# Kernel optimization log

Hardware: AMD Instinct MI355X
Metric: run time of the kernel (lower is better)

Reference implementation:

```python
import jax, jax.numpy as jnp
import numpy as np

A = 20000        # distinct library arcs
T = 500000       # timing arcs in design
S = 8            # LUT slew-axis length
C = 8            # LUT load-axis length
G = 250000       # gates
TOTAL_U = 1000000  # gate x candidate-master entries
SCALE = 1.0e15
MAX_CAP = 1.0e-12
MAX_ITER = 3


def _axis_interval(ax, x):
    """ax: [M,K] monotone axes, x: [M]. Returns lower index i0 in [0,K-2] and frac a (may extrapolate)."""
    K = ax.shape[1]
    i0 = jnp.clip(jnp.sum(ax <= x[:, None], axis=1) - 1, 0, K - 2)
    ar = jnp.arange(ax.shape[0])
    x0 = ax[ar, i0]
    x1 = ax[ar, i0 + 1]
    a = (x - x0) / (x1 - x0)
    return i0, a


def _bilinear_gate(in_slew, load, dtab, stab, axs, axc):
    """Batched bilinear interpolation into per-arc 2D LUTs. All leading dims M."""
    M = in_slew.shape[0]
    ar = jnp.arange(M)
    i0, a = _axis_interval(axs, in_slew)
    j0, b = _axis_interval(axc, load)
    i1, j1 = i0 + 1, j0 + 1

    def _blerp(t):
        return ((1 - a) * (1 - b) * t[ar, i0, j0]
                + (1 - a) * b * t[ar, i0, j1]
                + a * (1 - b) * t[ar, i1, j0]
                + a * b * t[ar, i1, j1])

    return _blerp(dtab), _blerp(stab)


def _compute_ceff_batch(in_slew, c1, c2, rpi, dtab, stab, axs, axc, max_iter=MAX_ITER):
    ceff = jnp.maximum(c1 + c2, 1e-30)
    for _ in range(max_iter):
        d, _ = _bilinear_gate(in_slew, ceff, dtab, stab, axs, axc)
        tau = jnp.maximum(d, 1e-30)
        ratio = jnp.minimum(2.0 * tau / jnp.maximum(in_slew, 1e-30), 10.0)
        h = jnp.where(ratio > 0.01, (1.0 - jnp.exp(-ratio)) / ratio, 1.0 - ratio / 2.0)
        ceff = jnp.maximum(c1 + c2 * h, 1e-30)
    return ceff


def _segment_softmax(logits, gate_id, num_groups):
    """Numerically stable per-gate softmax via segment reductions."""
    gmax = jax.ops.segment_max(logits, gate_id, num_segments=num_groups)
    ex = jnp.exp(logits - gmax[gate_id])
    gsum = jax.ops.segment_sum(ex, gate_id, num_segments=num_groups)
    return ex / gsum[gate_id]


def _gate_grouped_forward(in_arr, in_slew, c1, c2, rpi, arc_idx_r, arc_idx_f,
                          unateness, delay_table, slew_table, load_index, slew_index):
    t = arc_idx_r.shape[0]
    arc_flat = jnp.stack([arc_idx_r, arc_idx_f], axis=1).reshape(-1)  # [2T]
    una = unateness[arc_flat]
    is_fall = jnp.arange(2 * t, dtype=una.dtype) % 2
    rf_idx = (una ^ is_fall).reshape(t, 2)  # rise/fall select per column
    in_slew_sel = jnp.take_along_axis(in_slew, rf_idx, axis=1).reshape(-1)
    in_arr_sel = jnp.take_along_axis(in_arr, rf_idx, axis=1).reshape(-1)

    dtab = delay_table[arc_flat]   # [2T,S,C] big gather (memory bound)
    stab = slew_table[arc_flat]
    axc = load_index[arc_flat]     # [2T,C]
    axs = slew_index[arc_flat]     # [2T,S]

    c1_f = jnp.repeat(c1, 2) / SCALE
    c2_f = jnp.repeat(c2, 2) / SCALE
    rpi_f = jnp.repeat(rpi, 2)
    load = _compute_ceff_batch(in_slew_sel, c1_f, c2_f, rpi_f, dtab, stab, axs, axc)
    load = jnp.minimum(load, MAX_CAP)

    arc_delay, arc_slew = _bilinear_gate(in_slew_sel, load, dtab, stab, axs, axc)
    arr_out = (in_arr_sel + arc_delay).reshape(t, 2)
    slew_out = arc_slew.reshape(t, 2)
    return jnp.concatenate([arr_out, slew_out], axis=1)  # [T,4]


def setup_inputs() -> dict:
    key = jax.random.key(0)
    ks = jax.random.split(key, 14)
    U_flat = jax.random.normal(ks[0], (TOTAL_U,), jnp.float32)
    gate_id = jnp.sort(jax.random.randint(ks[1], (TOTAL_U,), 0, G, dtype=jnp.int32))
    in_arr = jax.random.normal(ks[2], (T, 2), jnp.float32)
    in_slew = jax.random.uniform(ks[3], (T, 2), jnp.float32, 0.05, 3.0)
    c1 = jax.random.uniform(ks[4], (T,), jnp.float32, 0.0, 1.0)
    c2 = jax.random.uniform(ks[5], (T,), jnp.float32, 0.0, 1.0)
    rpi = jax.random.uniform(ks[6], (T,), jnp.float32, 0.1, 1.0)
    arc_idx_r = jax.random.randint(ks[7], (T,), 0, A, dtype=jnp.int32)
    arc_idx_f = jax.random.randint(ks[8], (T,), 0, A, dtype=jnp.int32)
    unateness = jax.random.randint(ks[9], (A,), 0, 2, dtype=jnp.int32)
    delay_table = jax.random.uniform(ks[10], (A, S, C), jnp.float32, 0.01, 1.0)
    slew_table = jax.random.uniform(ks[11], (A, S, C), jnp.float32, 0.01, 1.0)
    # strictly increasing LUT axes: slew axis ~[0.05, 4], load axis ~[5e-17, 3e-15]
    slew_index = jnp.cumsum(jax.random.uniform(ks[12], (A, S), jnp.float32, 0.05, 0.6), axis=1)
    load_index = jnp.cumsum(jax.random.uniform(ks[13], (A, C), jnp.float32, 0.05, 0.6), axis=1) * 1e-15
    return dict(U_flat=U_flat, gate_id=gate_id, in_arr=in_arr, in_slew=in_slew,
                c1=c1, c2=c2, rpi=rpi, arc_idx_r=arc_idx_r, arc_idx_f=arc_idx_f,
                unateness=unateness, delay_table=delay_table, slew_table=slew_table,
                slew_index=slew_index, load_index=load_index)


def reference(U_flat, gate_id, in_arr, in_slew, c1, c2, rpi, arc_idx_r, arc_idx_f,
              unateness, delay_table, slew_table, slew_index, load_index):
    weights = _segment_softmax(U_flat, gate_id, G)  # per-gate soft master selection
    out = _gate_grouped_forward(in_arr, in_slew, c1, c2, rpi, arc_idx_r, arc_idx_f,
                                unateness, delay_table, slew_table, load_index, slew_index)
    return out, weights
```

## Files before the change

### kernel.cpp

```cpp
#include <hip/hip_runtime.h>

#define T_N 500000
#define U_N 1000000
#define G_N 250000
#define A_N 20000

#define SBLK 256
#define HALO 96

__device__ __forceinline__ float sel8(const float (&r)[8], int j) {
    float v = r[0];
#pragma unroll
    for (int k = 1; k < 8; ++k) v = (j >= k) ? r[k] : v;
    return v;
}

__device__ __forceinline__ void load8(const float* __restrict__ p, float (&r)[8]) {
    const float4* q = (const float4*)p;
    float4 a = q[0], b = q[1];
    r[0]=a.x; r[1]=a.y; r[2]=a.z; r[3]=a.w;
    r[4]=b.x; r[5]=b.y; r[6]=b.z; r[7]=b.w;
}


__global__ void __launch_bounds__(256)
softmax_lds_kernel(const float* __restrict__ U,
                   const int* __restrict__ gid,
                   float* __restrict__ wout) {
    __shared__ float se[SBLK + 2 * HALO];
    __shared__ int   sg[SBLK + 2 * HALO];

    int base = blockIdx.x * SBLK;
    int wstart = base - HALO;

    for (int k = threadIdx.x; k < SBLK + 2 * HALO; k += SBLK) {
        int idx = wstart + k;
        if (idx >= 0 && idx < U_N) {
            se[k] = expf(U[idx]);
            sg[k] = gid[idx];
        } else {
            se[k] = 0.0f;
            sg[k] = -1 - k;
        }
    }
    __syncthreads();

    int i = base + threadIdx.x;
    if (i >= U_N) return;

    int li = threadIdx.x + HALO;
    int g = sg[li];
    float mye = se[li];
    float s = mye;
    for (int j = li - 1; j >= 0 && sg[j] == g; --j) s += se[j];
    for (int j = li + 1; j < SBLK + 2 * HALO && sg[j] == g; ++j) s += se[j];

    wout[i] = mye / s;
}


__global__ void __launch_bounds__(256)
timing_kernel(const float2* __restrict__ in_arr,
              const float2* __restrict__ in_slew,
              const float* __restrict__ c1,
              const float* __restrict__ c2,
              const int* __restrict__ arc_r,
              const int* __restrict__ arc_f,
              const int* __restrict__ una,
              const float* __restrict__ dtab,
              const float* __restrict__ stab,
              const float* __restrict__ sidx,
              const float* __restrict__ lidx,
              float4* __restrict__ out)
{
    int t = blockIdx.x * blockDim.x + threadIdx.x;
    if (t >= T_N) return;

    float2 ia = in_arr[t];
    float2 is = in_slew[t];
    float c1f = c1[t] / 1.0e15f;
    float c2f = c2[t] / 1.0e15f;
    int arcs0 = arc_r[t];
    int arcs1 = arc_f[t];

    float res_arr[2], res_slew[2];

#pragma unroll
    for (int col = 0; col < 2; ++col) {
        int arc = (col == 0) ? arcs0 : arcs1;
        int u   = una[arc];
        int rf  = u ^ col;
        float slew = rf ? is.y : is.x;
        float arr  = rf ? ia.y : ia.x;

        float s[8], cx[8];
        load8(sidx + (size_t)arc * 8, s);
        load8(lidx + (size_t)arc * 8, cx);

        int cnt = 0;
#pragma unroll
        for (int k = 0; k < 8; ++k) cnt += (s[k] <= slew) ? 1 : 0;
        int i0 = min(max(cnt - 1, 0), 6);
        float x0 = sel8(s, i0);
        float x1 = sel8(s, i0 + 1);
        float a = (slew - x0) / (x1 - x0);
        float om_a = 1.0f - a;

        float d0[8], d1[8];
        load8(dtab + (size_t)arc * 64 + (size_t)i0 * 8, d0);
        load8(dtab + (size_t)arc * 64 + (size_t)i0 * 8 + 8, d1);

        float slew_den = fmaxf(slew, 1e-30f);
        float ceff = fmaxf(c1f + c2f, 1e-30f);
#pragma unroll
        for (int it = 0; it < 3; ++it) {
            int jc = 0;
#pragma unroll
            for (int k = 0; k < 8; ++k) jc += (cx[k] <= ceff) ? 1 : 0;
            int j0 = min(max(jc - 1, 0), 6);
            float y0 = sel8(cx, j0);
            float y1 = sel8(cx, j0 + 1);
            float b = (ceff - y0) / (y1 - y0);
            float om_b = 1.0f - b;
            float v00 = sel8(d0, j0), v01 = sel8(d0, j0 + 1);
            float v10 = sel8(d1, j0), v11 = sel8(d1, j0 + 1);
            float d = om_a * om_b * v00 + om_a * b * v01
                    + a * om_b * v10 + a * b * v11;
            float tau = fmaxf(d, 1e-30f);
            float ratio = fminf(2.0f * tau / slew_den, 10.0f);
            float h = (ratio > 0.01f) ? (1.0f - expf(-ratio)) / ratio
                                      : 1.0f - 0.5f * ratio;
            ceff = fmaxf(c1f + c2f * h, 1e-30f);
        }
        float load = fminf(ceff, 1.0e-12f);

        int jc = 0;
#pragma unroll
        for (int k = 0; k < 8; ++k) jc += (cx[k] <= load) ? 1 : 0;
        int j0 = min(max(jc - 1, 0), 6);
        float y0 = sel8(cx, j0);
        float y1 = sel8(cx, j0 + 1);
        float b = (load - y0) / (y1 - y0);
        float om_b = 1.0f - b;

        float v00 = sel8(d0, j0), v01 = sel8(d0, j0 + 1);
        float v10 = sel8(d1, j0), v11 = sel8(d1, j0 + 1);
        float delay = om_a * om_b * v00 + om_a * b * v01
                    + a * om_b * v10 + a * b * v11;

        const float* srow = stab + (size_t)arc * 64 + (size_t)i0 * 8;
        float s00 = srow[j0],     s01 = srow[j0 + 1];
        float s10 = srow[8 + j0], s11 = srow[8 + j0 + 1];
        float sl = om_a * om_b * s00 + om_a * b * s01
                 + a * om_b * s10 + a * b * s11;

        res_arr[col]  = arr + delay;
        res_slew[col] = sl;
    }

    out[t] = make_float4(res_arr[0], res_arr[1], res_slew[0], res_slew[1]);
}

extern "C" void kernel_launch(void* const* d_in, const int* in_sizes, int n_in,
                              void* d_out, int out_size, void* d_ws, size_t ws_size,
                              hipStream_t stream) {
    const float*  U      = (const float*)d_in[0];
    const int*    gid    = (const int*)d_in[1];
    const float2* in_arr = (const float2*)d_in[2];
    const float2* in_slw = (const float2*)d_in[3];
    const float*  c1     = (const float*)d_in[4];
    const float*  c2     = (const float*)d_in[5];
    const int*    arc_r  = (const int*)d_in[7];
    const int*    arc_f  = (const int*)d_in[8];
    const int*    una    = (const int*)d_in[9];
    const float*  dtab   = (const float*)d_in[10];
    const float*  stab   = (const float*)d_in[11];
    const float*  sidx   = (const float*)d_in[12];
    const float*  lidx   = (const float*)d_in[13];

    float* out  = (float*)d_out;
    float* wout = out + (size_t)T_N * 4;

    softmax_lds_kernel<<<(U_N + SBLK - 1) / SBLK, SBLK, 0, stream>>>(U, gid, wout);

    timing_kernel<<<(T_N + 255) / 256, 256, 0, stream>>>(
        in_arr, in_slw, c1, c2, arc_r, arc_f, una, dtab, stab, sidx, lidx,
        (float4*)out);
}
```

Before: 172.1 us.

## Sort timing arcs by library arc via histogram/scan/scatter before LUT evaluation

Adds a counting-sort pipeline (histogram, single-block scan, atomic scatter) that groups the 2T arc evaluations by library arc index and packs per-item inputs into a workspace. A new kernel then evaluates each item in sorted order, so neighbouring threads read the same LUT rows and gather-load locality improves. The cost is four extra launches, global atomics, a serial single-block scan, extra workspace traffic, and scattered 4-byte output writes. The original kernel is kept as a fallback when the workspace is too small.

```diff
diff --git a/kernel.cpp b/kernel.cpp
--- a/kernel.cpp
+++ b/kernel.cpp
@@ -4,6 +4,7 @@
 #define U_N 1000000
 #define G_N 250000
 #define A_N 20000
+#define ITEMS (2 * T_N)
 
 #define SBLK 256
 #define HALO 96
@@ -56,6 +57,161 @@
     for (int j = li + 1; j < SBLK + 2 * HALO && sg[j] == g; ++j) s += se[j];
 
     wout[i] = mye / s;
+}
+
+
+__global__ void hist_zero_kernel(int* __restrict__ hist) {
+    int i = blockIdx.x * blockDim.x + threadIdx.x;
+    if (i < A_N) hist[i] = 0;
+}
+
+__global__ void hist_kernel(const int* __restrict__ arc_r,
+                            const int* __restrict__ arc_f,
+                            int* __restrict__ hist) {
+    int i = blockIdx.x * blockDim.x + threadIdx.x;
+    if (i >= ITEMS) return;
+    int t = i >> 1;
+    int arc = (i & 1) ? arc_f[t] : arc_r[t];
+    atomicAdd(&hist[arc], 1);
+}
+
+__global__ void __launch_bounds__(1024)
+scan_kernel(const int* __restrict__ hist, int* __restrict__ ofs) {
+    __shared__ int part[1024];
+    const int CHUNK = (A_N + 1023) / 1024;
+    int tid = threadIdx.x;
+    int beg = tid * CHUNK;
+    int end = min(beg + CHUNK, A_N);
+    int s = 0;
+    for (int k = beg; k < end; ++k) s += hist[k];
+    part[tid] = s;
+    __syncthreads();
+    for (int off = 1; off < 1024; off <<= 1) {
+        int v = (tid >= off) ? part[tid - off] : 0;
+        __syncthreads();
+        part[tid] += v;
+        __syncthreads();
+    }
+    int run = (tid > 0) ? part[tid - 1] : 0;
+    for (int k = beg; k < end; ++k) { ofs[k] = run; run += hist[k]; }
+}
+
+__global__ void __launch_bounds__(256)
+scatter_kernel(const int* __restrict__ arc_r,
+               const int* __restrict__ arc_f,
+               const int* __restrict__ una,
+               const float2* __restrict__ in_arr,
+               const float2* __restrict__ in_slew,
+               const float* __restrict__ c1,
+               const float* __restrict__ c2,
+               int* __restrict__ ofs,
+               uint2* __restrict__ meta,
+               float4* __restrict__ vals) {
+    int i = blockIdx.x * blockDim.x + threadIdx.x;
+    if (i >= ITEMS) return;
+    int t   = i >> 1;
+    int col = i & 1;
+    int arc = col ? arc_f[t] : arc_r[t];
+    int pos = atomicAdd(&ofs[arc], 1);
+
+    float2 ia = in_arr[t];
+    float2 is = in_slew[t];
+    int rf = una[arc] ^ col;
+    float arr  = rf ? ia.y : ia.x;
+    float slew = rf ? is.y : is.x;
+    float c1f = c1[t] / 1.0e15f;
+    float c2f = c2[t] / 1.0e15f;
+
+    meta[pos] = make_uint2((unsigned)i, (unsigned)arc);
+    vals[pos] = make_float4(arr, slew, c1f, c2f);
+}
+
+
+__global__ void __launch_bounds__(256)
+timing_sorted_kernel(const uint2* __restrict__ meta,
+                     const float4* __restrict__ vals,
+                     const float* __restrict__ dtab,
+                     const float* __restrict__ stab,
+                     const float* __restrict__ sidx,
+                     const float* __restrict__ lidx,
+                     float* __restrict__ out) {
+    int p = blockIdx.x * blockDim.x + threadIdx.x;
+    if (p >= ITEMS) return;
+
+    uint2  m = meta[p];
+    float4 v = vals[p];
+    unsigned i   = m.x;
+    int      arc = (int)m.y;
+    float arr  = v.x;
+    float slew = v.y;
+    float c1f  = v.z;
+    float c2f  = v.w;
+
+    float s[8], cx[8];
+    load8(sidx + (size_t)arc * 8, s);
+    load8(lidx + (size_t)arc * 8, cx);
+
+    int cnt = 0;
+#pragma unroll
+    for (int k = 0; k < 8; ++k) cnt += (s[k] <= slew) ? 1 : 0;
+    int i0 = min(max(cnt - 1, 0), 6);
+    float x0 = sel8(s, i0);
+    float x1 = sel8(s, i0 + 1);
+    float a = (slew - x0) / (x1 - x0);
+    float om_a = 1.0f - a;
+
+    float d0[8], d1[8];
+    load8(dtab + (size_t)arc * 64 + (size_t)i0 * 8, d0);
+    load8(dtab + (size_t)arc * 64 + (size_t)i0 * 8 + 8, d1);
+
+    float slew_den = fmaxf(slew, 1e-30f);
+    float ceff = fmaxf(c1f + c2f, 1e-30f);
+#pragma unroll
+    for (int it = 0; it < 3; ++it) {
+        int jc = 0;
+#pragma unroll
+        for (int k = 0; k < 8; ++k) jc += (cx[k] <= ceff) ? 1 : 0;
+        int j0 = min(max(jc - 1, 0), 6);
+        float y0 = sel8(cx, j0);
+        float y1 = sel8(cx, j0 + 1);
+        float b = (ceff - y0) / (y1 - y0);
+        float om_b = 1.0f - b;
+        float v00 = sel8(d0, j0), v01 = sel8(d0, j0 + 1);
+        float v10 = sel8(d1, j0), v11 = sel8(d1, j0 + 1);
+        float d = om_a * om_b * v00 + om_a * b * v01
+                + a * om_b * v10 + a * b * v11;
+        float tau = fmaxf(d, 1e-30f);
+        float ratio = fminf(2.0f * tau / slew_den, 10.0f);
+        float h = (ratio > 0.01f) ? (1.0f - expf(-ratio)) / ratio
+                                  : 1.0f - 0.5f * ratio;
+        ceff = fmaxf(c1f + c2f * h, 1e-30f);
+    }
+    float load = fminf(ceff, 1.0e-12f);
+
+    int jc = 0;
+#pragma unroll
+    for (int k = 0; k < 8; ++k) jc += (cx[k] <= load) ? 1 : 0;
+    int j0 = min(max(jc - 1, 0), 6);
+    float y0 = sel8(cx, j0);
+    float y1 = sel8(cx, j0 + 1);
+    float b = (load - y0) / (y1 - y0);
+    float om_b = 1.0f - b;
+
+    float v00 = sel8(d0, j0), v01 = sel8(d0, j0 + 1);
+    float v10 = sel8(d1, j0), v11 = sel8(d1, j0 + 1);
+    float delay = om_a * om_b * v00 + om_a * b * v01
+                + a * om_b * v10 + a * b * v11;
+
+    const float* srow = stab + (size_t)arc * 64 + (size_t)i0 * 8;
+    float s00 = srow[j0],     s01 = srow[j0 + 1];
+    float s10 = srow[8 + j0], s11 = srow[8 + j0 + 1];
+    float sl = om_a * om_b * s00 + om_a * b * s01
+             + a * om_b * s10 + a * b * s11;
+
+    size_t t  = (size_t)(i >> 1);
+    int   col = (int)(i & 1);
+    out[t * 4 + col]     = arr + delay;
+    out[t * 4 + 2 + col] = sl;
 }
 
 
@@ -71,8 +227,7 @@
               const float* __restrict__ stab,
               const float* __restrict__ sidx,
               const float* __restrict__ lidx,
-              float4* __restrict__ out)
-{
+              float4* __restrict__ out) {
     int t = blockIdx.x * blockDim.x + threadIdx.x;
     if (t >= T_N) return;
 
@@ -183,7 +338,24 @@
 
     softmax_lds_kernel<<<(U_N + SBLK - 1) / SBLK, SBLK, 0, stream>>>(U, gid, wout);
 
-    timing_kernel<<<(T_N + 255) / 256, 256, 0, stream>>>(
-        in_arr, in_slw, c1, c2, arc_r, arc_f, una, dtab, stab, sidx, lidx,
-        (float4*)out);
-}
+    float4* vals = (float4*)d_ws;
+    uint2*  meta = (uint2*)((char*)d_ws + (size_t)ITEMS * sizeof(float4));
+    int*    hist = (int*)((char*)meta + (size_t)ITEMS * sizeof(uint2));
+    int*    ofs  = hist + A_N;
+    size_t need = (size_t)ITEMS * (sizeof(float4) + sizeof(uint2))
+                + (size_t)2 * A_N * sizeof(int);
+
+    if (ws_size >= need) {
+        hist_zero_kernel<<<(A_N + 255) / 256, 256, 0, stream>>>(hist);
+        hist_kernel<<<(ITEMS + 255) / 256, 256, 0, stream>>>(arc_r, arc_f, hist);
+        scan_kernel<<<1, 1024, 0, stream>>>(hist, ofs);
+        scatter_kernel<<<(ITEMS + 255) / 256, 256, 0, stream>>>(
+            arc_r, arc_f, una, in_arr, in_slw, c1, c2, ofs, meta, vals);
+        timing_sorted_kernel<<<(ITEMS + 255) / 256, 256, 0, stream>>>(
+            meta, vals, dtab, stab, sidx, lidx, out);
+    } else {
+        timing_kernel<<<(T_N + 255) / 256, 256, 0, stream>>>(
+            in_arr, in_slw, c1, c2, arc_r, arc_f, una, dtab, stab, sidx, lidx,
+            (float4*)out);
+    }
+}
```

Measured after the change: 338.9 us. +96.9%, slower.
